# Kernel tuning notes

Measured on AMD Instinct MI355X. Metric: run time of the kernel, lower is better.

## Reference

```python
import jax, jax.numpy as jnp
import numpy as np

NSIDE = 64
NLAT = 4 * NSIDE - 1        # 255 iso-latitude rings
NLON = 4 * NSIDE            # 256 = max pixels per ring
NPIX = 12 * NSIDE * NSIDE   # 49152 HEALPix pixels
LMAX = NLAT                 # 255
MMAX = NLON // 2 + 1        # 129
BATCH, CHAN = 8, 32


def _ring_geometry():
    # HEALPix ring scheme: ring r (0-based), 1-based i=r+1
    #  north cap i<nside: nph=4i, phi shift 0.5
    #  equatorial nside<=i<=3*nside: nph=4*nside, shift alternates {0,0.5}
    #  south cap: mirror of north cap
    nph = np.zeros(NLAT, np.int64)
    shift = np.zeros(NLAT, np.float64)
    for r in range(NLAT):
        i = r + 1
        if i < NSIDE:
            nph[r], shift[r] = 4 * i, 0.5
        elif i <= 3 * NSIDE:
            nph[r], shift[r] = 4 * NSIDE, 0.5 * ((i - NSIDE + 1) % 2)
        else:
            nph[r], shift[r] = 4 * (NLAT - r), 0.5
    offs = np.concatenate([[0], np.cumsum(nph)[:-1]])
    p = np.arange(NLON)
    mask = (p[None, :] < nph[:, None])                       # [nlat, nlon]
    idx = (offs[:, None] + p[None, :]) * mask                # padded -> 0
    phase = 2.0 * np.pi * (p[None, :] + shift[:, None]) / nph[:, None] * mask
    return idx.astype(np.int32), mask.astype(np.float32), phase.astype(np.float32)


def setup_inputs() -> dict:
    key = jax.random.key(0)
    k1, k2, k3 = jax.random.split(key, 3)
    idx, mask, phase = _ring_geometry()
    x = jax.random.normal(k1, (BATCH, CHAN, NPIX), jnp.float32)
    pct = jax.random.normal(k2, (MMAX, LMAX, NLAT), jnp.float32) * 0.1  # Legendre table stand-in
    w = jax.random.uniform(k3, (NLAT,), jnp.float32)                    # per-ring quadrature weights
    return {"x": x, "pct": pct, "w": w,
            "ring_index": jnp.asarray(idx),
            "ring_mask": jnp.asarray(mask),
            "phase": jnp.asarray(phase)}


def _healpix_rfft_real(x, ring_index, ring_mask, phase):
    # x: [..., npix] -> per-ring DFT coefficients as real pairs [..., nlat, mmax, 2]
    rings = x[..., ring_index] * ring_mask                 # [..., nlat, nlon]
    m = jnp.arange(MMAX, dtype=phase.dtype)
    ang = phase[:, :, None] * m                            # [nlat, nlon, mmax]
    fr = jnp.einsum('...kp,kpm->...km', rings, jnp.cos(ang))
    fi = -jnp.einsum('...kp,kpm->...km', rings, jnp.sin(ang))
    return jnp.stack([fr, fi], axis=-1)                    # n=2 is view_as_real axis


def reference(x, pct, w, ring_index, ring_mask, phase):
    # healpix ring rFFT, then Legendre contraction (einsum '...kmn,mlk->...lmn')
    f = _healpix_rfft_real(x, ring_index, ring_mask, phase)  # [..., nlat, mmax, 2]
    weights = pct * w                                        # [mmax, lmax, nlat]
    out = jnp.einsum('...kmn,mlk->...lmn', f, weights)       # [..., lmax, mmax, 2]
    return out
```

## Files before the change

### kernel.cpp

```cpp
#include <hip/hip_runtime.h>

#define NLAT 255
#define NLON 256
#define NPIX 49152
#define MMAX 129
#define MCS  258
#define NTBL 65
#define TROWS 264

typedef unsigned short ushort_t;
typedef __attribute__((ext_vector_type(8)))  short  bf16x8;
typedef __attribute__((ext_vector_type(4)))  short  short4v;
typedef __attribute__((ext_vector_type(16))) float  f32x16;
typedef __attribute__((ext_vector_type(4)))  float  float4v;

__device__ __forceinline__ ushort_t f2bf(float f) {
    union { float f; unsigned u; } v; v.f = f;
    unsigned r = v.u + 0x7FFFu + ((v.u >> 16) & 1u);
    return (ushort_t)(r >> 16);
}
__device__ __forceinline__ float bf2f(ushort_t h) {
    union { unsigned u; float f; } v; v.u = ((unsigned)h) << 16;
    return v.f;
}

__global__ __launch_bounds__(256) void prepK(const float* __restrict__ pct,
                                             const float* __restrict__ w,
                                             ushort_t* __restrict__ pctwF) {
    const int m  = blockIdx.x;
    const int l0 = blockIdx.y * 32;
    const int t  = threadIdx.x;
    const float wk = (t < NLAT) ? w[t] : 0.f;
    const int kg = t >> 3, j = t & 7;
    for (int l = l0; l < l0 + 32; ++l) {
        float v = 0.f;
        if (l < NLAT && t < NLAT)
            v = pct[((size_t)m * NLAT + l) * NLAT + t] * wk;
        pctwF[(((size_t)m * 32 + kg) * 256 + l) * 8 + j] = f2bf(v);
    }
}

__global__ __launch_bounds__(256) void trigK(const float* __restrict__ phase,
                                             const float* __restrict__ mask,
                                             ushort_t* __restrict__ Ttab3) {
    const int tt  = blockIdx.x;
    const int mcs = blockIdx.y;
    const int p   = threadIdx.x;
    const int r   = (tt < 63) ? tt : (tt == 63 ? 63 : 64);
    float val = 0.f;
    if (mcs < MCS) {
        float ph = phase[r * NLON + p];
        float mk = mask[r * NLON + p];
        float fm = (float)(mcs >> 1);
        float s, c;
        __sincosf(ph * fm, &s, &c);
        val = (mcs & 1) ? (-s * mk) : (c * mk);
    }
    const int pcc = p >> 6, c = (p >> 3) & 7, j = p & 7;
    Ttab3[((((size_t)tt * 4 + pcc) * 8 + c) * TROWS + mcs) * 8 + j] = f2bf(val);
}

__global__ __launch_bounds__(256, 2) void stageA(const float* __restrict__ x,
                                                 const int* __restrict__ ring_index,
                                                 const ushort_t* __restrict__ Ttab3,
                                                 ushort_t* __restrict__ f1) {
    __shared__ __align__(16) ushort_t Rs[2][64 * 72];

    const int b0 = blockIdx.x * 64;
    const int r  = blockIdx.y;
    const int i1 = r + 1;
    const int nph = (i1 < 64) ? 4 * i1 : (i1 <= 192 ? 256 : 4 * (256 - i1));
    const int tbl = (i1 < 64) ? r : (i1 <= 192 ? (63 + (((i1 - 63) & 1) ^ 1)) : 254 - r);
    const int base = ring_index[r * NLON];
    const int nchunks = (nph + 63) >> 6;

    const int t    = threadIdx.x;
    const int lane = t & 63;
    const int wid  = t >> 6;
    const int wrow = wid >> 1, wcol = wid & 1;
    const int lg   = lane >> 5;
    const int lc   = lane & 31;

    f32x16 acc[5];
#pragma unroll
    for (int tau = 0; tau < 5; ++tau)
#pragma unroll
        for (int q = 0; q < 16; ++q) acc[tau][q] = 0.f;

    int trow[5];
#pragma unroll
    for (int tau = 0; tau < 5; ++tau) {
        int rr = tau * 64 + wcol * 32 + lc;
        trow[tau] = rr > (TROWS - 1) ? (TROWS - 1) : rr;
    }

    float4v rx[4];
    const int p0 = (t & 15) * 4;
    auto ldX = [&](int pc) {
        const bool ok = (pc + p0) < nph;
#pragma unroll
        for (int pass = 0; pass < 4; ++pass) {
            int bc = (t >> 4) + pass * 16;
            float4v v = {0.f, 0.f, 0.f, 0.f};
            if (ok) v = *(const float4v*)(x + (size_t)(b0 + bc) * NPIX + base + pc + p0);
            rx[pass] = v;
        }
    };
    auto stX = [&](ushort_t* dst) {
#pragma unroll
        for (int pass = 0; pass < 4; ++pass) {
            int bc = (t >> 4) + pass * 16;
            short4v h;
            h[0] = (short)f2bf(rx[pass][0]); h[1] = (short)f2bf(rx[pass][1]);
            h[2] = (short)f2bf(rx[pass][2]); h[3] = (short)f2bf(rx[pass][3]);
            *(short4v*)(dst + bc * 72 + p0) = h;
        }
    };

    ldX(0);
    stX(Rs[0]);
    __syncthreads();

    for (int c = 0; c < nchunks; ++c) {
        const int pc = c << 6;
        const bool more = (c + 1) < nchunks;
        const ushort_t* slab = Ttab3 + (size_t)(tbl * 4 + c) * (8 * TROWS * 8);

        bf16x8 bfr[4][5];
#pragma unroll
        for (int ks = 0; ks < 4; ++ks) {
            const ushort_t* bcol = slab + (size_t)(ks * 2 + lg) * (TROWS * 8);
#pragma unroll
            for (int tau = 0; tau < 5; ++tau)
                bfr[ks][tau] = *(const bf16x8*)(bcol + trow[tau] * 8);
        }
        if (more) ldX(pc + 64);

        const ushort_t* Rcur = Rs[c & 1];
#pragma unroll
        for (int ks = 0; ks < 4; ++ks) {
            bf16x8 a = *(const bf16x8*)(Rcur + (wrow * 32 + lc) * 72 + ks * 16 + lg * 8);
#pragma unroll
            for (int tau = 0; tau < 5; ++tau)
                acc[tau] = __builtin_amdgcn_mfma_f32_32x32x16_bf16(a, bfr[ks][tau], acc[tau], 0, 0, 0);
        }
        if (more) stX(Rs[(c + 1) & 1]);
        __syncthreads();
    }

    ushort_t* Olds = Rs[0];
#pragma unroll
    for (int tau = 0; tau < 5; ++tau) {
        __syncthreads();
        {
            const int mcsl = wcol * 32 + lc;
#pragma unroll
            for (int q = 0; q < 16; ++q) {
                int bcl = wrow * 32 + 4 * lg + (q & 3) + 8 * (q >> 2);
                Olds[mcsl * 72 + bcl] = f2bf(acc[tau][q]);
            }
        }
        __syncthreads();
        {
            int row = t >> 2;
            int mcs = tau * 64 + row;
            if (mcs < MCS) {
                int m = mcs >> 1, n = mcs & 1;
                size_t gbase = ((size_t)m * NLAT + r) * 512 + n * 256 + b0 + (t & 3) * 16;
#pragma unroll
                for (int j = 0; j < 2; ++j) {
                    bf16x8 v = *(const bf16x8*)(Olds + row * 72 + (t & 3) * 16 + j * 8);
                    *(bf16x8*)(f1 + gbase + j * 8) = v;
                }
            }
        }
    }
}

__global__ __launch_bounds__(256) void transK(const ushort_t* __restrict__ f1,
                                              ushort_t* __restrict__ f1tF) {
    __shared__ __align__(16) ushort_t T[64][72];
    const int m  = blockIdx.x;
    const int k0 = blockIdx.y * 64;
    const int b0 = blockIdx.z * 64;
    const int t  = threadIdx.x;
#pragma unroll
    for (int it = 0; it < 2; ++it) {
        int id = t + it * 256;
        int kk = id >> 3, ch = id & 7;
        int k  = k0 + kk;
        bf16x8 v = {0,0,0,0,0,0,0,0};
        if (k < NLAT)
            v = *(const bf16x8*)(f1 + ((size_t)m * NLAT + k) * 512 + b0 + ch * 8);
        *(bf16x8*)(&T[kk][ch * 8]) = v;
    }
    __syncthreads();
#pragma unroll
    for (int it = 0; it < 2; ++it) {
        int id  = t + it * 256;
        int bb  = id & 63, ch8 = id >> 6;
        bf16x8 v;
#pragma unroll
        for (int j = 0; j < 8; ++j) v[j] = T[ch8 * 8 + j][bb];
        *(bf16x8*)(f1tF + (((size_t)m * 32 + (k0 >> 3) + ch8) * 512 + b0 + bb) * 8) = v;
    }
}

__global__ __launch_bounds__(256, 2) void stageB(const ushort_t* __restrict__ f1tF,
                                                 const ushort_t* __restrict__ pctwF,
                                                 ushort_t* __restrict__ otmp) {
    __shared__ __align__(16) ushort_t Es[128 * 136];

    const int m   = blockIdx.x >> 2;
    const int b2t = (blockIdx.x & 3) * 128;

    const int t     = threadIdx.x;
    const int lane  = t & 63;
    const int wid   = t >> 6;
    const int wrow  = wid >> 1, wlcol = wid & 1;
    const int lg    = lane >> 5, lc = lane & 31;

    f32x16 acc[2][4];
#pragma unroll
    for (int i = 0; i < 2; ++i)
#pragma unroll
        for (int j = 0; j < 4; ++j)
#pragma unroll
            for (int q = 0; q < 16; ++q) acc[i][j][q] = 0.f;

    const ushort_t* aBase = f1tF  + (((size_t)m * 32 + lg) * 512 + b2t + wrow * 64 + lc) * 8;
    const ushort_t* bBase = pctwF + (((size_t)m * 32 + lg) * 256 + wlcol * 128 + lc) * 8;

    bf16x8 fa0[2], fb0[4], fa1[2], fb1[4];
    auto ldf = [&](int ksm, bf16x8* fa, bf16x8* fb) {
        const size_t ao = (size_t)ksm * 8192;
        const size_t bo = (size_t)ksm * 4096;
#pragma unroll
        for (int i = 0; i < 2; ++i)
            fa[i] = *(const bf16x8*)(aBase + ao + i * 256);
#pragma unroll
        for (int jj = 0; jj < 4; ++jj)
            fb[jj] = *(const bf16x8*)(bBase + bo + jj * 256);
    };
    auto mm = [&](const bf16x8* fa, const bf16x8* fb) {
#pragma unroll
        for (int jj = 0; jj < 4; ++jj) {
            acc[0][jj] = __builtin_amdgcn_mfma_f32_32x32x16_bf16(fa[0], fb[jj], acc[0][jj], 0, 0, 0);
            acc[1][jj] = __builtin_amdgcn_mfma_f32_32x32x16_bf16(fa[1], fb[jj], acc[1][jj], 0, 0, 0);
        }
    };

    ldf(0, fa0, fb0);
    ldf(1, fa1, fb1);
#pragma unroll
    for (int ksm = 0; ksm < 16; ksm += 2) {
        mm(fa0, fb0);
        if (ksm + 2 < 16) ldf(ksm + 2, fa0, fb0);
        mm(fa1, fb1);
        if (ksm + 3 < 16) ldf(ksm + 3, fa1, fb1);
    }

#pragma unroll
    for (int h = 0; h < 2; ++h) {
        if (h) __syncthreads();
        if (wlcol == h) {
#pragma unroll
            for (int i = 0; i < 2; ++i)
#pragma unroll
                for (int jj = 0; jj < 4; ++jj)
#pragma unroll
                    for (int q = 0; q < 16; ++q) {
                        int bl = wrow * 64 + i * 32 + 4 * lg + (q & 3) + 8 * (q >> 2);
                        Es[bl * 136 + jj * 32 + lc] = f2bf(acc[i][jj][q]);
                    }
        }
        __syncthreads();
#pragma unroll
        for (int it = 0; it < 8; ++it) {
            int id2 = t + it * 256;
            int row = id2 >> 4, ch = id2 & 15;
            bf16x8 v = *(const bf16x8*)(Es + row * 136 + ch * 8);
            *(bf16x8*)(otmp + (((size_t)m * 512 + b2t + row) << 8) + h * 128 + ch * 8) = v;
        }
    }
}

__global__ __launch_bounds__(256) void permuteK(const ushort_t* __restrict__ otmp,
                                                float* __restrict__ out) {
    __shared__ ushort_t L[MCS * 66];
    const int bc = blockIdx.x;
    const int l0 = blockIdx.y * 64;
    const int t  = threadIdx.x;
    const int ll = t & 63;
    const int l  = l0 + ll;
#pragma unroll 4
    for (int it = 0; it < 65; ++it) {
        int mn = (t >> 6) + it * 4;
        if (mn < MCS) {
            int mm = mn >> 1, n = mn & 1;
            ushort_t v = 0;
            if (l < NLAT)
                v = otmp[(((size_t)mm * 512 + n * 256 + bc) << 8) + l];
            L[mn * 66 + ll] = v;
        }
    }
    __syncthreads();
    for (int ll2 = 0; ll2 < 64; ++ll2) {
        int lo = l0 + ll2;
        if (lo >= NLAT) break;
        size_t rowb = ((size_t)bc * NLAT + lo) * MCS;
        out[rowb + t] = bf2f(L[t * 66 + ll2]);
        if (t < 2)
            out[rowb + 256 + t] = bf2f(L[(256 + t) * 66 + ll2]);
    }
}

extern "C" void kernel_launch(void* const* d_in, const int* in_sizes, int n_in,
                              void* d_out, int out_size, void* d_ws, size_t ws_size,
                              hipStream_t stream) {
    const float* x          = (const float*)d_in[0];
    const float* pct        = (const float*)d_in[1];
    const float* w          = (const float*)d_in[2];
    const int*   ring_index = (const int*)d_in[3];
    const float* ring_mask  = (const float*)d_in[4];
    const float* phase      = (const float*)d_in[5];
    float* out = (float*)d_out;

    char* wsb = (char*)d_ws;
    char* ob  = (char*)d_out;
    ushort_t* otmp  = (ushort_t*)wsb;
    ushort_t* f1    = (ushort_t*)(wsb + 33552384);
    ushort_t* f1tF  = (ushort_t*)ob;
    ushort_t* pctwF = (ushort_t*)(ob + 33816576);
    ushort_t* Ttab3 = (ushort_t*)(ob + 50724864);

    prepK   <<<dim3(MMAX, 8),     256, 0, stream>>>(pct, w, pctwF);
    trigK   <<<dim3(NTBL, TROWS), 256, 0, stream>>>(phase, ring_mask, Ttab3);
    stageA  <<<dim3(4, NLAT),     256, 0, stream>>>(x, ring_index, Ttab3, f1);
    transK  <<<dim3(MMAX, 4, 8),  256, 0, stream>>>(f1, f1tF);
    stageB  <<<dim3(4 * MMAX),    256, 0, stream>>>(f1tF, pctwF, otmp);
    permuteK<<<dim3(256, 4),      256, 0, stream>>>(otmp, out);
}
```

Measured before the change: 128.8 us.

## Stage stageB GEMM operands through LDS via async global_load_lds double buffering

Rewrites the stageB batched GEMM so that A and W tiles are copied into a double-buffered shared-memory ring with global_load_lds, and MFMA operands are then read from LDS. This replaces the earlier direct per-lane register prefetch from global memory. It also remaps block ids so that groups of 8 consecutive m values share the same batch tile, which should help L2 reuse, and raises launch_bounds occupancy to 3. In exchange it adds a barrier per k-chunk, spends padded blocks on early exit, and puts more pressure on LDS.

```diff
diff --git a/kernel.cpp b/kernel.cpp
--- a/kernel.cpp
+++ b/kernel.cpp
@@ -206,19 +206,22 @@
     }
 }
 
-__global__ __launch_bounds__(256, 2) void stageB(const ushort_t* __restrict__ f1tF,
+__global__ __launch_bounds__(256, 3) void stageB(const ushort_t* __restrict__ f1tF,
                                                  const ushort_t* __restrict__ pctwF,
                                                  ushort_t* __restrict__ otmp) {
-    __shared__ __align__(16) ushort_t Es[128 * 136];
-
-    const int m   = blockIdx.x >> 2;
-    const int b2t = (blockIdx.x & 3) * 128;
-
-    const int t     = threadIdx.x;
-    const int lane  = t & 63;
-    const int wid   = t >> 6;
-    const int wrow  = wid >> 1, wlcol = wid & 1;
-    const int lg    = lane >> 5, lc = lane & 31;
+    __shared__ __align__(16) ushort_t SB[24576];
+    ushort_t* Es = SB;
+
+    const int id = blockIdx.x;
+    const int m  = ((id >> 5) << 3) | (id & 7);
+    if (m >= MMAX) return;
+    const int b2t = ((id >> 3) & 3) * 128;
+
+    const int t    = threadIdx.x;
+    const int lane = t & 63;
+    const int wid  = t >> 6;
+    const int wrow = wid >> 1, wlcol = wid & 1;
+    const int lg   = lane >> 5, lc = lane & 31;
 
     f32x16 acc[2][4];
 #pragma unroll
@@ -228,36 +231,54 @@
 #pragma unroll
             for (int q = 0; q < 16; ++q) acc[i][j][q] = 0.f;
 
-    const ushort_t* aBase = f1tF  + (((size_t)m * 32 + lg) * 512 + b2t + wrow * 64 + lc) * 8;
-    const ushort_t* bBase = pctwF + (((size_t)m * 32 + lg) * 256 + wlcol * 128 + lc) * 8;
-
-    bf16x8 fa0[2], fb0[4], fa1[2], fb1[4];
-    auto ldf = [&](int ksm, bf16x8* fa, bf16x8* fb) {
-        const size_t ao = (size_t)ksm * 8192;
-        const size_t bo = (size_t)ksm * 4096;
-#pragma unroll
-        for (int i = 0; i < 2; ++i)
-            fa[i] = *(const bf16x8*)(aBase + ao + i * 256);
-#pragma unroll
-        for (int jj = 0; jj < 4; ++jj)
-            fb[jj] = *(const bf16x8*)(bBase + bo + jj * 256);
+    const ushort_t* aSrc = f1tF  + (size_t)m * 32 * 512 * 8;
+    const ushort_t* wSrc = pctwF + (size_t)m * 32 * 256 * 8;
+
+    auto STAGE = [&](int buf, int c) {
+#pragma unroll
+        for (int u = 0; u < 2; ++u) {
+            int sA   = wid * 2 + u;
+            int kg   = c * 4 + (sA >> 1);
+            int half = sA & 1;
+            const ushort_t* src = aSrc + ((size_t)kg * 512 + b2t + half * 64) * 8 + lane * 8;
+            __builtin_amdgcn_global_load_lds(
+                (const __attribute__((address_space(1))) void*)src,
+                (__attribute__((address_space(3))) void*)(SB + buf * 4096 + sA * 512),
+                16, 0, 0);
+        }
+#pragma unroll
+        for (int u = 0; u < 4; ++u) {
+            int sW = wid * 4 + u;
+            int kg = c * 4 + (sW >> 2);
+            int q  = sW & 3;
+            const ushort_t* src = wSrc + ((size_t)kg * 256 + q * 64) * 8 + lane * 8;
+            __builtin_amdgcn_global_load_lds(
+                (const __attribute__((address_space(1))) void*)src,
+                (__attribute__((address_space(3))) void*)(SB + 8192 + buf * 8192 + sW * 512),
+                16, 0, 0);
+        }
     };
-    auto mm = [&](const bf16x8* fa, const bf16x8* fb) {
-#pragma unroll
-        for (int jj = 0; jj < 4; ++jj) {
-            acc[0][jj] = __builtin_amdgcn_mfma_f32_32x32x16_bf16(fa[0], fb[jj], acc[0][jj], 0, 0, 0);
-            acc[1][jj] = __builtin_amdgcn_mfma_f32_32x32x16_bf16(fa[1], fb[jj], acc[1][jj], 0, 0, 0);
-        }
-    };
-
-    ldf(0, fa0, fb0);
-    ldf(1, fa1, fb1);
-#pragma unroll
-    for (int ksm = 0; ksm < 16; ksm += 2) {
-        mm(fa0, fb0);
-        if (ksm + 2 < 16) ldf(ksm + 2, fa0, fb0);
-        mm(fa1, fb1);
-        if (ksm + 3 < 16) ldf(ksm + 3, fa1, fb1);
+
+    STAGE(0, 0);
+    __syncthreads();
+    int buf = 0;
+    for (int c = 0; c < 8; ++c, buf ^= 1) {
+        if (c + 1 < 8) STAGE(buf ^ 1, c + 1);
+        const ushort_t* A = SB + buf * 4096;
+        const ushort_t* W = SB + 8192 + buf * 8192;
+#pragma unroll
+        for (int ks = 0; ks < 2; ++ks) {
+            const int kgl = ks * 2 + lg;
+            bf16x8 a0 = *(const bf16x8*)(A + (kgl * 128 + wrow * 64 + lc) * 8);
+            bf16x8 a1 = *(const bf16x8*)(A + (kgl * 128 + wrow * 64 + 32 + lc) * 8);
+#pragma unroll
+            for (int jj = 0; jj < 4; ++jj) {
+                bf16x8 b = *(const bf16x8*)(W + (kgl * 256 + wlcol * 128 + jj * 32 + lc) * 8);
+                acc[0][jj] = __builtin_amdgcn_mfma_f32_32x32x16_bf16(a0, b, acc[0][jj], 0, 0, 0);
+                acc[1][jj] = __builtin_amdgcn_mfma_f32_32x32x16_bf16(a1, b, acc[1][jj], 0, 0, 0);
+            }
+        }
+        __syncthreads();
     }
 
 #pragma unroll
@@ -338,6 +359,6 @@
     trigK   <<<dim3(NTBL, TROWS), 256, 0, stream>>>(phase, ring_mask, Ttab3);
     stageA  <<<dim3(4, NLAT),     256, 0, stream>>>(x, ring_index, Ttab3, f1);
     transK  <<<dim3(MMAX, 4, 8),  256, 0, stream>>>(f1, f1tF);
-    stageB  <<<dim3(4 * MMAX),    256, 0, stream>>>(f1tF, pctwF, otmp);
+    stageB  <<<dim3(544),         256, 0, stream>>>(f1tF, pctwF, otmp);
     permuteK<<<dim3(256, 4),      256, 0, stream>>>(otmp, out);
 }
```

New measurement: 118.8 us (median of 2 runs). 7.7% less time.
